# Performance work log

Measured on AMD Instinct MI355X. Metric: run time of the kernel, lower is better.

The kernel has to match this reference:

```python
import jax, jax.numpy as jnp
import numpy as np

T, B, D, H = 512, 64, 512, 512


def setup_inputs() -> dict:
    key = jax.random.key(0)
    k0, k1, k2, k3 = jax.random.split(key, 4)
    inputs = jax.random.normal(k0, (T, B, D), dtype=jnp.float32)
    # weight_norm params per gate: v [H, D+H], g [H], b [H]; gates stacked as [4, ...]
    v = jax.random.normal(k1, (4, H, D + H), dtype=jnp.float32) * 0.05
    g = jax.random.uniform(k2, (4, H), dtype=jnp.float32, minval=0.5, maxval=1.5)
    b = jax.random.normal(k3, (4, H), dtype=jnp.float32) * 0.01
    return {"inputs": inputs, "v": v, "g": g, "b": b}


def reference(inputs, v, g, b):
    # weight_norm (dim=0): W[o,:] = g[o] * v[o,:] / ||v[o,:]||
    norm = jnp.sqrt(jnp.sum(v * v, axis=-1, keepdims=True))  # [4,H,1]
    W = v * (g[..., None] / norm)                             # [4,H,D+H]
    # fuse 4 gate GEMMs into one: order f, i, u(g), o
    W_all = W.reshape(4 * H, D + H)                           # [4H, D+H]
    b_all = b.reshape(4 * H)                                  # [4H]
    hd = inputs.shape[-1] - 0  # D known statically

    def step(carry, x):
        hx, cx = carry
        combined = jnp.concatenate([x, hx], axis=1)           # [B, D+H]
        z = combined @ W_all.T + b_all                        # [B, 4H]
        f, i, u, o = jnp.split(z, 4, axis=1)
        f = jax.nn.sigmoid(f)
        i = jax.nn.sigmoid(i)
        u = jnp.tanh(u)
        o = jax.nn.sigmoid(o)
        cx = f * cx + i * u
        hx = o * jnp.tanh(cx)
        return (hx, cx), hx

    Bsz = inputs.shape[1]
    h0 = jnp.zeros((Bsz, H), dtype=inputs.dtype)
    c0 = jnp.zeros((Bsz, H), dtype=inputs.dtype)
    (hx, cx), outputs = jax.lax.scan(step, (h0, c0), inputs)
    return outputs, hx, cx
```

## Files before the change

### kernel.cpp

```cpp
#include <hip/hip_runtime.h>
#include <hip/hip_bf16.h>
#include <stdint.h>

typedef unsigned short u16;
typedef unsigned int u32;
typedef unsigned long long u64;
typedef float f32x4 __attribute__((ext_vector_type(4)));
typedef short s16x8 __attribute__((ext_vector_type(8)));

#define T_STEPS 512
#define NBATCH 64
#define NHID 512
#define NCOLS 2048
#define KIN 1024

__device__ __forceinline__ u16 f2bf(float f) {
  uint32_t u = __builtin_bit_cast(uint32_t, f);
  u += 0x7FFFu + ((u >> 16) & 1u);
  return (u16)(u >> 16);
}
__device__ __forceinline__ float bf2f(u16 u) {
  uint32_t v = ((uint32_t)u) << 16;
  return __builtin_bit_cast(float, v);
}
__device__ __forceinline__ void gload_lds16(const void* g, void* l) {
  __builtin_amdgcn_global_load_lds(
      (const __attribute__((address_space(1))) unsigned int*)g,
      (__attribute__((address_space(3))) unsigned int*)l, 16, 0, 0);
}

__global__ void k_prep_w(const float* __restrict__ v, const float* __restrict__ g,
                         u16* __restrict__ Wx, u16* __restrict__ Wh) {
  const int row = blockIdx.x * 4 + (threadIdx.x >> 6);
  const int lane = threadIdx.x & 63;
  const float* vr = v + (size_t)row * KIN;
  float ss = 0.f;
#pragma unroll
  for (int c = 0; c < 4; ++c) {
    float4 q = *reinterpret_cast<const float4*>(vr + lane * 16 + c * 4);
    ss += q.x * q.x + q.y * q.y + q.z * q.z + q.w * q.w;
  }
#pragma unroll
  for (int off = 1; off < 64; off <<= 1) ss += __shfl_xor(ss, off);
  const float scale = g[row] / sqrtf(ss);

  s16x8 o;
  const float* src = vr + lane * 8;
#pragma unroll
  for (int i = 0; i < 8; ++i) o[i] = (short)f2bf(src[i] * scale);
  *reinterpret_cast<s16x8*>(Wx + (size_t)row * 512 + lane * 8) = o;
  const float* src2 = vr + 512 + lane * 8;
#pragma unroll
  for (int i = 0; i < 8; ++i) o[i] = (short)f2bf(src2[i] * scale);
  *reinterpret_cast<s16x8*>(Wh + (size_t)row * 512 + lane * 8) = o;
}

__global__ void k_cvt_x(const float* __restrict__ x, u16* __restrict__ xb) {
  const size_t i = (size_t)blockIdx.x * blockDim.x + threadIdx.x;
  float4 a = *reinterpret_cast<const float4*>(x + i * 8);
  float4 b = *reinterpret_cast<const float4*>(x + i * 8 + 4);
  s16x8 o;
  o[0] = (short)f2bf(a.x); o[1] = (short)f2bf(a.y);
  o[2] = (short)f2bf(a.z); o[3] = (short)f2bf(a.w);
  o[4] = (short)f2bf(b.x); o[5] = (short)f2bf(b.y);
  o[6] = (short)f2bf(b.z); o[7] = (short)f2bf(b.w);
  *reinterpret_cast<s16x8*>(xb + i * 8) = o;
}

__global__ __launch_bounds__(256) void k_gemm_xz(
    const u16* __restrict__ A, const u16* __restrict__ B,
    const float* __restrict__ bias, u16* __restrict__ C) {
  __shared__ u16 As[128 * 64];
  __shared__ u16 Bs[128 * 64];
  const int tid = threadIdx.x;
  const int w = tid >> 6, l = tid & 63;
  const int l15 = l & 15, lhi = l >> 4;
  const int m0 = blockIdx.x * 128, n0 = blockIdx.y * 128;
  const int wm = (w & 1) * 64, wn = (w >> 1) * 64;
  f32x4 acc[4][4];
#pragma unroll
  for (int i = 0; i < 4; ++i)
#pragma unroll
    for (int j = 0; j < 4; ++j) acc[i][j] = (f32x4){0.f, 0.f, 0.f, 0.f};

  for (int kk = 0; kk < 8; ++kk) {
    const int kt = kk * 64;
#pragma unroll
    for (int is = 0; is < 4; ++is) {
      const int p = is * 4096 + tid * 16;
      const int row = p >> 7, cb = p & 127;
      gload_lds16((const char*)A + (size_t)(m0 + row) * 1024 + kt * 2 + cb,
                  (char*)As + p);
      gload_lds16((const char*)B + (size_t)(n0 + row) * 1024 + kt * 2 + cb,
                  (char*)Bs + p);
    }
    __syncthreads();
#pragma unroll
    for (int ks = 0; ks < 2; ++ks) {
      s16x8 af[4], bf[4];
#pragma unroll
      for (int mt = 0; mt < 4; ++mt)
        af[mt] = *reinterpret_cast<const s16x8*>(
            (const char*)As + (wm + mt * 16 + l15) * 128 + ks * 64 + lhi * 16);
#pragma unroll
      for (int nt = 0; nt < 4; ++nt)
        bf[nt] = *reinterpret_cast<const s16x8*>(
            (const char*)Bs + (wn + nt * 16 + l15) * 128 + ks * 64 + lhi * 16);
#pragma unroll
      for (int mt = 0; mt < 4; ++mt)
#pragma unroll
        for (int nt = 0; nt < 4; ++nt)
          acc[mt][nt] = __builtin_amdgcn_mfma_f32_16x16x32_bf16(
              af[mt], bf[nt], acc[mt][nt], 0, 0, 0);
    }
    __syncthreads();
  }
#pragma unroll
  for (int nt = 0; nt < 4; ++nt) {
    const int n = n0 + wn + nt * 16 + l15;
    const float bb = bias[n];
#pragma unroll
    for (int mt = 0; mt < 4; ++mt)
#pragma unroll
      for (int r = 0; r < 4; ++r) {
        const int m = m0 + wm + mt * 16 + lhi * 4 + r;
        C[(size_t)m * 2048 + n] = f2bf(acc[mt][nt][r] + bb);
      }
  }
}

__global__ __launch_bounds__(256, 1) void k_rec(
    const u16* __restrict__ Wh, const u16* __restrict__ xz,
    u16* __restrict__ h_g, u32* __restrict__ bar,
    float* __restrict__ out) {
  const int blk = blockIdx.x;
  const int grp = blockIdx.y;
  const int tid = threadIdx.x;
  const int gate = tid >> 6;
  const int l = tid & 63;
  const int l15 = l & 15, lhi = l >> 4;
  const int hid0 = blk * 16;

  __shared__ u16 hbuf[16 * 520];
  __shared__ float zbuf[4][16][17];

  s16x8 bfrag[16];
  {
    const u16* wr = Wh + (size_t)(gate * 512 + hid0 + l15) * 512;
#pragma unroll
    for (int ks = 0; ks < 16; ++ks)
      bfrag[ks] = *reinterpret_cast<const s16x8*>(wr + ks * 32 + lhi * 8);
  }

  const int j2 = tid & 15;
  const int m2 = tid >> 4;
  float creg = 0.f, hlast = 0.f;
  u32* myflags = bar + grp * 32;

  for (int t = 0; t < T_STEPS; ++t) {
    if (t > 0) {
      const u32 tgt = (u32)t;
      bool ready = false;
      for (int it = 0; it < 50000 && !ready; ++it) {
        u32 fv = __hip_atomic_load(myflags + (l & 31), __ATOMIC_RELAXED,
                                   __HIP_MEMORY_SCOPE_AGENT);
        ready = __all(fv >= tgt);
      }
    }

    u64* hg = (u64*)h_g + (size_t)(t & 1) * 8192;
#pragma unroll
    for (int j = 0; j < 8; ++j) {
      const int q = tid + 256 * j;
      const int row = q >> 7, cu = q & 127;
      u64 vq = __hip_atomic_load(hg + (size_t)(grp * 16 + row) * 128 + cu,
                                 __ATOMIC_RELAXED, __HIP_MEMORY_SCOPE_AGENT);
      *reinterpret_cast<u64*>(hbuf + row * 520 + cu * 4) = vq;
    }
    const u16* xp = xz + (size_t)(t * 64 + grp * 16) * 2048 + gate * 512 + hid0 + l15;
    float xv[4];
#pragma unroll
    for (int r = 0; r < 4; ++r) xv[r] = bf2f(xp[(size_t)(lhi * 4 + r) * 2048]);

    __syncthreads();

    f32x4 acc0 = {0.f, 0.f, 0.f, 0.f}, acc1 = {0.f, 0.f, 0.f, 0.f};
#pragma unroll
    for (int ks = 0; ks < 16; ks += 2) {
      s16x8 a0 = *reinterpret_cast<const s16x8*>(hbuf + l15 * 520 + ks * 32 + lhi * 8);
      s16x8 a1 = *reinterpret_cast<const s16x8*>(hbuf + l15 * 520 + (ks + 1) * 32 + lhi * 8);
      acc0 = __builtin_amdgcn_mfma_f32_16x16x32_bf16(a0, bfrag[ks], acc0, 0, 0, 0);
      acc1 = __builtin_amdgcn_mfma_f32_16x16x32_bf16(a1, bfrag[ks + 1], acc1, 0, 0, 0);
    }
    const f32x4 acc = acc0 + acc1;
#pragma unroll
    for (int r = 0; r < 4; ++r) zbuf[gate][lhi * 4 + r][l15] = acc[r] + xv[r];
    __syncthreads();

    const float zf = zbuf[0][m2][j2];
    const float zi = zbuf[1][m2][j2];
    const float zu = zbuf[2][m2][j2];
    const float zo = zbuf[3][m2][j2];
    const float ff = 1.f / (1.f + __expf(-zf));
    const float ii = 1.f / (1.f + __expf(-zi));
    const float uu = 1.f - 2.f / (__expf(2.f * zu) + 1.f);
    const float oo = 1.f / (1.f + __expf(-zo));
    creg = ff * creg + ii * uu;
    const float hn = oo * (1.f - 2.f / (__expf(2.f * creg) + 1.f));
    hlast = hn;

    const u32 hv = f2bf(hn);
    const u32 nb = (u32)__shfl_down((int)hv, 1);
    if ((l & 1) == 0) {
      const u32 packed = hv | (nb << 16);
      u32* dst = (u32*)h_g + (size_t)((t + 1) & 1) * 16384 +
                 (((size_t)(grp * 16 + m2) * 512 + hid0 + j2) >> 1);
      __hip_atomic_store(dst, packed, __ATOMIC_RELAXED, __HIP_MEMORY_SCOPE_AGENT);
    }

    __syncthreads();
    if (tid == 0)
      __hip_atomic_store(myflags + blk, (u32)(t + 1), __ATOMIC_RELAXED,
                         __HIP_MEMORY_SCOPE_AGENT);
    out[((size_t)t * 64 + grp * 16 + m2) * 512 + hid0 + j2] = hn;
  }

  float* hxp = out + (size_t)T_STEPS * 64 * 512;
  float* cxp = hxp + 64 * 512;
  hxp[(size_t)(grp * 16 + m2) * 512 + hid0 + j2] = hlast;
  cxp[(size_t)(grp * 16 + m2) * 512 + hid0 + j2] = creg;
}

extern "C" void kernel_launch(void* const* d_in, const int* in_sizes, int n_in,
                              void* d_out, int out_size, void* d_ws, size_t ws_size,
                              hipStream_t stream) {
  const float* x = (const float*)d_in[0];
  const float* v = (const float*)d_in[1];
  const float* g = (const float*)d_in[2];
  const float* b = (const float*)d_in[3];
  float* out = (float*)d_out;

  char* ws = (char*)d_ws;
  const size_t SZ_W = 2048ull * 512 * 2;
  u16* Wx = (u16*)(ws);
  u16* Wh = (u16*)(ws + SZ_W);
  u16* xb = (u16*)(ws + 2 * SZ_W);
  u16* xz = (u16*)(ws + 2 * SZ_W + 32768ull * 512 * 2);
  char* hb = ws + 2 * SZ_W + 32768ull * 512 * 2 + 32768ull * 2048 * 2;
  u16* h_g = (u16*)hb;
  u32* bar = (u32*)(hb + 131072);

  hipMemsetAsync(hb, 0, 131072 + 1024, stream);
  k_prep_w<<<512, 256, 0, stream>>>(v, g, Wx, Wh);
  k_cvt_x<<<8192, 256, 0, stream>>>(x, xb);
  k_gemm_xz<<<dim3(256, 16), 256, 0, stream>>>(xb, Wx, b, xz);
  k_rec<<<dim3(32, 4), 256, 0, stream>>>(Wh, xz, h_g, bar, out);
}
```

Before: 2.110 ms.

## Replace flag barrier with per-element step-tagged hidden-state words in recurrence

The recurrent kernel no longer writes h and then sets a per-block flag that consumers spin on. Each hidden value is now stored as a 32-bit word holding the bf16 value and a 16-bit step tag. Consumers poll the words directly until every tag matches the current step, then unpack the values into LDS. This removes the extra __syncthreads, the flag round trip and the separate reload from the critical path of each step. In exchange the h traffic doubles and every spin iteration re-reads the whole 16x512 slice.

Result: slower. 2.262 ms (+7.2%).

```diff
diff --git a/kernel.cpp b/kernel.cpp
--- a/kernel.cpp
+++ b/kernel.cpp
@@ -7,6 +7,7 @@
 typedef unsigned long long u64;
 typedef float f32x4 __attribute__((ext_vector_type(4)));
 typedef short s16x8 __attribute__((ext_vector_type(8)));
+typedef unsigned int u32x2 __attribute__((ext_vector_type(2)));
 
 #define T_STEPS 512
 #define NBATCH 64
@@ -131,8 +132,7 @@
 
 __global__ __launch_bounds__(256, 1) void k_rec(
     const u16* __restrict__ Wh, const u16* __restrict__ xz,
-    u16* __restrict__ h_g, u32* __restrict__ bar,
-    float* __restrict__ out) {
+    u32* __restrict__ htag, float* __restrict__ out) {
   const int blk = blockIdx.x;
   const int grp = blockIdx.y;
   const int tid = threadIdx.x;
@@ -155,33 +155,42 @@
   const int j2 = tid & 15;
   const int m2 = tid >> 4;
   float creg = 0.f, hlast = 0.f;
-  u32* myflags = bar + grp * 32;
 
   for (int t = 0; t < T_STEPS; ++t) {
-    if (t > 0) {
-      const u32 tgt = (u32)t;
-      bool ready = false;
-      for (int it = 0; it < 50000 && !ready; ++it) {
-        u32 fv = __hip_atomic_load(myflags + (l & 31), __ATOMIC_RELAXED,
-                                   __HIP_MEMORY_SCOPE_AGENT);
-        ready = __all(fv >= tgt);
-      }
-    }
-
-    u64* hg = (u64*)h_g + (size_t)(t & 1) * 8192;
-#pragma unroll
-    for (int j = 0; j < 8; ++j) {
-      const int q = tid + 256 * j;
-      const int row = q >> 7, cu = q & 127;
-      u64 vq = __hip_atomic_load(hg + (size_t)(grp * 16 + row) * 128 + cu,
-                                 __ATOMIC_RELAXED, __HIP_MEMORY_SCOPE_AGENT);
-      *reinterpret_cast<u64*>(hbuf + row * 520 + cu * 4) = vq;
-    }
     const u16* xp = xz + (size_t)(t * 64 + grp * 16) * 2048 + gate * 512 + hid0 + l15;
     float xv[4];
 #pragma unroll
     for (int r = 0; r < 4; ++r) xv[r] = bf2f(xp[(size_t)(lhi * 4 + r) * 2048]);
 
+    const u32* hslot = htag + (size_t)(t & 1) * 32768 + (size_t)grp * 8192;
+    const u32 tg = (u32)t & 0xffffu;
+    u32 vals[8][4];
+    bool done = false;
+    for (int it = 0; it < 20000 && !done; ++it) {
+#pragma unroll
+      for (int v = 0; v < 8; ++v) {
+        const u32* p = hslot + (v * 256 + tid) * 4;
+#pragma unroll
+        for (int j = 0; j < 4; ++j)
+          vals[v][j] = __hip_atomic_load(p + j, __ATOMIC_RELAXED,
+                                         __HIP_MEMORY_SCOPE_AGENT);
+      }
+      done = true;
+#pragma unroll
+      for (int v = 0; v < 8; ++v)
+#pragma unroll
+        for (int j = 0; j < 4; ++j)
+          done = done && ((vals[v][j] & 0xffffu) == tg);
+    }
+#pragma unroll
+    for (int v = 0; v < 8; ++v) {
+      const int c = v * 256 + tid;
+      const int row = c >> 7, col4 = (c & 127) * 4;
+      u32x2 w2;
+      w2[0] = (vals[v][0] >> 16) | (vals[v][1] & 0xffff0000u);
+      w2[1] = (vals[v][2] >> 16) | (vals[v][3] & 0xffff0000u);
+      *reinterpret_cast<u32x2*>(&hbuf[row * 520 + col4]) = w2;
+    }
     __syncthreads();
 
     f32x4 acc0 = {0.f, 0.f, 0.f, 0.f}, acc1 = {0.f, 0.f, 0.f, 0.f};
@@ -209,19 +218,11 @@
     const float hn = oo * (1.f - 2.f / (__expf(2.f * creg) + 1.f));
     hlast = hn;
 
-    const u32 hv = f2bf(hn);
-    const u32 nb = (u32)__shfl_down((int)hv, 1);
-    if ((l & 1) == 0) {
-      const u32 packed = hv | (nb << 16);
-      u32* dst = (u32*)h_g + (size_t)((t + 1) & 1) * 16384 +
-                 (((size_t)(grp * 16 + m2) * 512 + hid0 + j2) >> 1);
-      __hip_atomic_store(dst, packed, __ATOMIC_RELAXED, __HIP_MEMORY_SCOPE_AGENT);
-    }
-
-    __syncthreads();
-    if (tid == 0)
-      __hip_atomic_store(myflags + blk, (u32)(t + 1), __ATOMIC_RELAXED,
-                         __HIP_MEMORY_SCOPE_AGENT);
+    const u32 pv = ((u32)f2bf(hn) << 16) | ((u32)(t + 1) & 0xffffu);
+    u32* dst = htag + (size_t)((t + 1) & 1) * 32768 +
+               (size_t)(grp * 16 + m2) * 512 + hid0 + j2;
+    __hip_atomic_store(dst, pv, __ATOMIC_RELAXED, __HIP_MEMORY_SCOPE_AGENT);
+
     out[((size_t)t * 64 + grp * 16 + m2) * 512 + hid0 + j2] = hn;
   }
 
@@ -247,12 +248,11 @@
   u16* xb = (u16*)(ws + 2 * SZ_W);
   u16* xz = (u16*)(ws + 2 * SZ_W + 32768ull * 512 * 2);
   char* hb = ws + 2 * SZ_W + 32768ull * 512 * 2 + 32768ull * 2048 * 2;
-  u16* h_g = (u16*)hb;
-  u32* bar = (u32*)(hb + 131072);
-
-  hipMemsetAsync(hb, 0, 131072 + 1024, stream);
+  u32* htag = (u32*)hb;
+
+  hipMemsetAsync(hb, 0, 262144, stream);
   k_prep_w<<<512, 256, 0, stream>>>(v, g, Wx, Wh);
   k_cvt_x<<<8192, 256, 0, stream>>>(x, xb);
   k_gemm_xz<<<dim3(256, 16), 256, 0, stream>>>(xb, Wx, b, xz);
-  k_rec<<<dim3(32, 4), 256, 0, stream>>>(Wh, xz, h_g, bar, out);
-}
+  k_rec<<<dim3(32, 4), 256, 0, stream>>>(Wh, xz, htag, out);
+}
```
